# Kernel optimization log

Hardware: AMD Instinct MI355X
Metric: run time of the kernel (lower is better)

The kernel has to match this reference:

```python
import jax, jax.numpy as jnp
import numpy as np

N, E = 50000, 800000
IN, HID, LAT = 512, 256, 128


def setup_inputs() -> dict:
    key = jax.random.key(0)
    ks = jax.random.split(key, 9)
    x = jax.random.normal(ks[0], (N, IN), dtype=jnp.float32)
    edge_index = jax.random.randint(ks[1], (2, E), 0, N, dtype=jnp.int64)
    edge_attr = jax.random.uniform(ks[2], (E,), dtype=jnp.float32)
    # GCNConv weights (glorot-ish scaling) and biases
    W1 = jax.random.normal(ks[3], (IN, HID), dtype=jnp.float32) / np.sqrt(IN)
    b1 = jnp.zeros((HID,), dtype=jnp.float32)
    W_mu = jax.random.normal(ks[4], (HID, LAT), dtype=jnp.float32) / np.sqrt(HID)
    b_mu = jnp.zeros((LAT,), dtype=jnp.float32)
    W_lv = jax.random.normal(ks[5], (HID, LAT), dtype=jnp.float32) / np.sqrt(HID)
    b_lv = jnp.zeros((LAT,), dtype=jnp.float32)
    return {"x": x, "edge_index": edge_index, "edge_attr": edge_attr,
            "W1": W1, "b1": b1, "W_mu": W_mu, "b_mu": b_mu,
            "W_lv": W_lv, "b_lv": b_lv}


def _gcn_norm(edge_index, edge_attr, num_nodes):
    # GCNConv default: add self-loops (weight 1), symmetric normalization
    loops = jnp.arange(num_nodes, dtype=edge_index.dtype)
    src = jnp.concatenate([edge_index[0], loops])
    dst = jnp.concatenate([edge_index[1], loops])
    w = jnp.concatenate([edge_attr, jnp.ones((num_nodes,), edge_attr.dtype)])
    deg = jax.ops.segment_sum(w, dst, num_segments=num_nodes)
    dis = jnp.where(deg > 0, jax.lax.rsqrt(jnp.maximum(deg, 1e-12)), 0.0)
    norm = dis[src] * w * dis[dst]  # [E + N]
    return src, dst, norm


def reference(x, edge_index, edge_attr, W1, b1, W_mu, b_mu, W_lv, b_lv):
    num_nodes = x.shape[0]
    src, dst, norm = _gcn_norm(edge_index, edge_attr, num_nodes)

    def conv(h, W, b):
        m = h @ W                      # dense transform [N, out]
        msg = m[src] * norm[:, None]   # gather + scale  [E+N, out]
        return jax.ops.segment_sum(msg, dst, num_segments=num_nodes) + b

    hidden = jax.nn.relu(conv(x, W1, b1))
    # Dropout(0.2) is identity in eval mode
    mu = conv(hidden, W_mu, b_mu)
    logvar = conv(hidden, W_lv, b_lv)
    return (mu, logvar)
```

## Files before the change

kernel.cpp:

```cpp
#include <hip/hip_runtime.h>

#define IN_F 512
#define HID_F 256
#define LAT_F 128

typedef __bf16 bf16x8 __attribute__((ext_vector_type(8)));
typedef float floatx4 __attribute__((ext_vector_type(4)));

#define FIX_SCALE 1048576.0f

__device__ __forceinline__ unsigned short f2bf(float f) {
    union { float f; unsigned u; } v; v.f = f;
    unsigned r = (v.u + 0x7fff + ((v.u >> 16) & 1)) >> 16;
    return (unsigned short)r;
}
__device__ __forceinline__ float bf2f(unsigned short h) {
    union { unsigned u; float f; } v; v.u = ((unsigned)h) << 16;
    return v.f;
}

__device__ __forceinline__ void gload_lds16(const void* g, void* lds) {
    __builtin_amdgcn_global_load_lds(
        (const __attribute__((address_space(1))) unsigned int*)(uintptr_t)g,
        (__attribute__((address_space(3))) unsigned int*)(uintptr_t)lds,
        16, 0, 0);
}


__global__ void prep_all(const float* __restrict__ W1, const float* __restrict__ Wmu,
                         const float* __restrict__ Wlv, unsigned long long* __restrict__ packed,
                         unsigned short* __restrict__ W1t, unsigned short* __restrict__ B2t,
                         int N) {
    int t = blockIdx.x * 256 + threadIdx.x;
    if (t < N) packed[t] = (1ULL << 32) | (unsigned long long)(unsigned)FIX_SCALE;
    if (t < HID_F * IN_F) {
        int n = t >> 9, k = t & 511;
        W1t[t] = f2bf(W1[(size_t)k * HID_F + n]);
    }
    if (t < HID_F * HID_F) {
        int n = t >> 8, k = t & 255;
        float v = (n < 128) ? Wmu[(size_t)k * LAT_F + n] : Wlv[(size_t)k * LAT_F + (n - 128)];
        B2t[t] = f2bf(v);
    }
}


__global__ void edge_deg(const int* __restrict__ ei, const float* __restrict__ attr,
                         unsigned long long* __restrict__ packed, int* __restrict__ slot, int E) {
    int e = blockIdx.x * 256 + threadIdx.x;
    if (e < E) {
        int d = ei[E + e];
        unsigned fw = __float2uint_rn(attr[e] * FIX_SCALE);
        unsigned long long old = atomicAdd(&packed[d], (1ULL << 32) | (unsigned long long)fw);
        slot[e] = (int)(old >> 32);
    }
}

__global__ void node_dis(const unsigned long long* __restrict__ packed,
                         float* __restrict__ dis, int* __restrict__ counts, int N) {
    int i = blockIdx.x * 256 + threadIdx.x;
    if (i < N) {
        unsigned long long p = packed[i];
        counts[i] = (int)(p >> 32);
        float dg = (float)(unsigned)(p & 0xffffffffu) * (1.0f / FIX_SCALE);
        dis[i] = dg > 0.f ? rsqrtf(fmaxf(dg, 1e-12f)) : 0.f;
    }
}


__global__ void scan_blocks(const int* __restrict__ counts, int* __restrict__ excl,
                            int* __restrict__ blockSums, int N) {
    __shared__ int sdata[256];
    int tid = threadIdx.x;
    int base = blockIdx.x * 1024 + tid * 4;
    int v[4]; int sum = 0;
#pragma unroll
    for (int j = 0; j < 4; ++j) { v[j] = (base + j < N) ? counts[base + j] : 0; sum += v[j]; }
    sdata[tid] = sum;
    __syncthreads();
    for (int off = 1; off < 256; off <<= 1) {
        int t = (tid >= off) ? sdata[tid - off] : 0;
        __syncthreads();
        sdata[tid] += t;
        __syncthreads();
    }
    if (tid == 255) blockSums[blockIdx.x] = sdata[255];
    int run = sdata[tid] - sum;
#pragma unroll
    for (int j = 0; j < 4; ++j) { if (base + j < N) excl[base + j] = run; run += v[j]; }
}

__global__ void scan_sums(int* blockSums, int NB) {
    __shared__ int s[64];
    int tid = threadIdx.x;
    int v = (tid < NB) ? blockSums[tid] : 0;
    s[tid] = v;
    __syncthreads();
    for (int off = 1; off < 64; off <<= 1) {
        int t = (tid >= off) ? s[tid - off] : 0;
        __syncthreads();
        s[tid] += t;
        __syncthreads();
    }
    if (tid < NB) blockSums[tid] = s[tid] - v;
}

__global__ void scan_add(int* row_ptr, const int* __restrict__ blockSums, int N, int total) {
    int tid = threadIdx.x;
    int base = blockIdx.x * 1024 + tid * 4;
    int add = blockSums[blockIdx.x];
#pragma unroll
    for (int j = 0; j < 4; ++j) if (base + j < N) row_ptr[base + j] += add;
    if (blockIdx.x == 0 && tid == 0) row_ptr[N] = total;
}


__global__ void fill_csr(const int* __restrict__ ei, const float* __restrict__ attr,
                         const int* __restrict__ slot, const float* __restrict__ dis,
                         const int* __restrict__ row_ptr,
                         int* __restrict__ col, float* __restrict__ val, int E, int N) {
    int e = blockIdx.x * 256 + threadIdx.x;
    if (e >= E + N) return;
    int s, d, sl; float w;
    if (e < E) { s = ei[e]; d = ei[E + e]; w = attr[e]; sl = slot[e]; }
    else       { s = d = e - E; w = 1.0f; sl = 0; }
    int pos = row_ptr[d] + sl;
    col[pos] = s;
    val[pos] = dis[s] * w * dis[d];
}


template <bool ABF16>
__global__ __launch_bounds__(256) void gemm_mfma(const void* __restrict__ Avoid,
                                                 const unsigned short* __restrict__ Bt,
                                                 unsigned short* __restrict__ C,
                                                 int M, int K) {
    __shared__ unsigned short As[64 * 32];
    __shared__ unsigned short Bs[256 * 32];
    int tid = threadIdx.x;
    int wave = tid >> 6, lane = tid & 63;
    int mrow = lane & 15, quad = lane >> 4;
    int blockRow = blockIdx.x * 64;

    floatx4 acc[4][4];
#pragma unroll
    for (int i = 0; i < 4; ++i)
#pragma unroll
        for (int j = 0; j < 4; ++j) acc[i][j] = (floatx4){0.f, 0.f, 0.f, 0.f};

    int r = tid >> 2;
    int kq = tid & 3;
    int arow = blockRow + r; if (arow >= M) arow = M - 1;

    unsigned short* AsWaveBase = &As[wave * 512];

    for (int k0 = 0; k0 < K; k0 += 32) {
        if constexpr (ABF16) {
            const unsigned short* A = (const unsigned short*)Avoid;
            gload_lds16(A + (size_t)arow * K + k0 + kq * 8, AsWaveBase);
        } else {
            const float* A = (const float*)Avoid;
            const float* p = A + (size_t)arow * K + k0 + kq * 8;
            float4 a0 = *(const float4*)p, a1 = *(const float4*)(p + 4);
            unsigned short h[8] = {f2bf(a0.x), f2bf(a0.y), f2bf(a0.z), f2bf(a0.w),
                                   f2bf(a1.x), f2bf(a1.y), f2bf(a1.z), f2bf(a1.w)};
            *(uint4*)&As[r * 32 + kq * 8] = *(uint4*)h;
        }
#pragma unroll
        for (int pass = 0; pass < 4; ++pass) {
            int bcol = r + pass * 64;
            gload_lds16(Bt + (size_t)bcol * K + k0 + kq * 8,
                        &Bs[(pass * 256 + wave * 64) * 8]);
        }
        __syncthreads();
        bf16x8 af[4];
#pragma unroll
        for (int i = 0; i < 4; ++i)
            af[i] = *(const bf16x8*)&As[(i * 16 + mrow) * 32 + quad * 8];
#pragma unroll
        for (int j = 0; j < 4; ++j) {
            bf16x8 bf = *(const bf16x8*)&Bs[(wave * 64 + j * 16 + mrow) * 32 + quad * 8];
#pragma unroll
            for (int i = 0; i < 4; ++i)
                acc[i][j] = __builtin_amdgcn_mfma_f32_16x16x32_bf16(af[i], bf, acc[i][j], 0, 0, 0);
        }
        __syncthreads();
    }
#pragma unroll
    for (int i = 0; i < 4; ++i)
#pragma unroll
        for (int j = 0; j < 4; ++j) {
            int colo = wave * 64 + j * 16 + mrow;
#pragma unroll
            for (int v = 0; v < 4; ++v) {
                int row = blockRow + i * 16 + quad * 4 + v;
                if (row < M) C[(size_t)row * HID_F + colo] = f2bf(acc[i][j][v]);
            }
        }
}


__global__ void agg_relu(const unsigned short* __restrict__ m, const int* __restrict__ row_ptr,
                         const int* __restrict__ col, const float* __restrict__ val,
                         const float* __restrict__ bias, unsigned short* __restrict__ hidden) {
    int i = blockIdx.x, l = threadIdx.x, c0 = l << 2;
    int p0 = row_ptr[i], p1 = row_ptr[i + 1];
    float a0 = 0.f, a1 = 0.f, a2 = 0.f, a3 = 0.f;
    for (int p = p0; p < p1; ++p) {
        int s = col[p]; float w = val[p];
        ushort4 u = *(const ushort4*)(m + (size_t)s * HID_F + c0);
        a0 = fmaf(bf2f(u.x), w, a0);
        a1 = fmaf(bf2f(u.y), w, a1);
        a2 = fmaf(bf2f(u.z), w, a2);
        a3 = fmaf(bf2f(u.w), w, a3);
    }
    float4 b = *(const float4*)(bias + c0);
    a0 = fmaxf(a0 + b.x, 0.f); a1 = fmaxf(a1 + b.y, 0.f);
    a2 = fmaxf(a2 + b.z, 0.f); a3 = fmaxf(a3 + b.w, 0.f);
    ushort4 o = make_ushort4(f2bf(a0), f2bf(a1), f2bf(a2), f2bf(a3));
    *(ushort4*)(hidden + (size_t)i * HID_F + c0) = o;
}

__global__ void agg_out(const unsigned short* __restrict__ m, const int* __restrict__ row_ptr,
                        const int* __restrict__ col, const float* __restrict__ val,
                        const float* __restrict__ bmu, const float* __restrict__ blv,
                        float* __restrict__ out, int N) {
    int i = blockIdx.x, l = threadIdx.x, c0 = l << 2;
    int p0 = row_ptr[i], p1 = row_ptr[i + 1];
    float a0 = 0.f, a1 = 0.f, a2 = 0.f, a3 = 0.f;
    for (int p = p0; p < p1; ++p) {
        int s = col[p]; float w = val[p];
        ushort4 u = *(const ushort4*)(m + (size_t)s * HID_F + c0);
        a0 = fmaf(bf2f(u.x), w, a0);
        a1 = fmaf(bf2f(u.y), w, a1);
        a2 = fmaf(bf2f(u.z), w, a2);
        a3 = fmaf(bf2f(u.w), w, a3);
    }
    if (l < 32) {
        float4 b = *(const float4*)(bmu + c0);
        float4 o = make_float4(a0 + b.x, a1 + b.y, a2 + b.z, a3 + b.w);
        *(float4*)(out + (size_t)i * LAT_F + c0) = o;
    } else {
        int c = c0 - 128;
        float4 b = *(const float4*)(blv + c);
        float4 o = make_float4(a0 + b.x, a1 + b.y, a2 + b.z, a3 + b.w);
        *(float4*)(out + (size_t)(N + i) * LAT_F + c) = o;
    }
}


extern "C" void kernel_launch(void* const* d_in, const int* in_sizes, int n_in,
                              void* d_out, int out_size, void* d_ws, size_t ws_size,
                              hipStream_t stream) {
    const float* x    = (const float*)d_in[0];
    const int*   ei   = (const int*)d_in[1];
    const float* attr = (const float*)d_in[2];
    const float* W1   = (const float*)d_in[3];
    const float* b1   = (const float*)d_in[4];
    const float* Wmu  = (const float*)d_in[5];
    const float* bmu  = (const float*)d_in[6];
    const float* Wlv  = (const float*)d_in[7];
    const float* blv  = (const float*)d_in[8];
    float* out = (float*)d_out;

    const int N  = in_sizes[0] / IN_F;
    const int E  = in_sizes[2];
    const int EN = E + N;

    char* w = (char*)d_ws;
    size_t off = 0;
    auto carve = [&](size_t bytes) -> void* {
        void* p = w + off; off += (bytes + 255) & ~(size_t)255; return p;
    };
    unsigned long long* packed = (unsigned long long*)carve((size_t)N * 8);
    float*          dis       = (float*)carve((size_t)N * 4);
    int*            counts    = (int*)  carve((size_t)N * 4);
    int*            row_ptr   = (int*)  carve((size_t)(N + 1) * 4);
    int*            blockSums = (int*)  carve(64 * 4);
    int*            slot      = (int*)  carve((size_t)E * 4);
    int*            col       = (int*)  carve((size_t)EN * 4);
    float*          val       = (float*)carve((size_t)EN * 4);
    unsigned short* W1t       = (unsigned short*)carve((size_t)HID_F * IN_F * 2);
    unsigned short* B2t       = (unsigned short*)carve((size_t)HID_F * HID_F * 2);
    unsigned short* m         = (unsigned short*)carve((size_t)N * HID_F * 2);
    unsigned short* hidden    = (unsigned short*)carve((size_t)N * HID_F * 2);

    prep_all<<<(HID_F * IN_F + 255) / 256, 256, 0, stream>>>(W1, Wmu, Wlv, packed, W1t, B2t, N);

    edge_deg<<<(E + 255) / 256, 256, 0, stream>>>(ei, attr, packed, slot, E);
    node_dis<<<(N + 255) / 256, 256, 0, stream>>>(packed, dis, counts, N);

    int NB = (N + 1023) / 1024;
    scan_blocks<<<NB, 256, 0, stream>>>(counts, row_ptr, blockSums, N);
    scan_sums<<<1, 64, 0, stream>>>(blockSums, NB);
    scan_add<<<NB, 256, 0, stream>>>(row_ptr, blockSums, N, EN);

    fill_csr<<<(EN + 255) / 256, 256, 0, stream>>>(ei, attr, slot, dis, row_ptr, col, val, E, N);

    int gblocks = (N + 63) / 64;
    gemm_mfma<false><<<gblocks, 256, 0, stream>>>(x, W1t, m, N, IN_F);
    agg_relu<<<N, 64, 0, stream>>>(m, row_ptr, col, val, b1, hidden);
    gemm_mfma<true><<<gblocks, 256, 0, stream>>>(hidden, B2t, m, N, HID_F);
    agg_out<<<N, 64, 0, stream>>>(m, row_ptr, col, val, bmu, blv, out, N);
}
```

Before: 440.0 us.

## Double-buffer GEMM LDS tiles and fold node_dis into scan_blocks

The MFMA GEMM now uses two LDS buffers, so the next K-slice is prefetched while the current one is consumed, which cuts one barrier per iteration. In the fp32-A path the global loads are issued early and converted to bf16 after the MFMAs, to hide load latency. Separately, the node_dis kernel is removed and its degree-to-rsqrt and count extraction work is folded into scan_blocks, dropping one launch and the counts buffer. Doubling LDS raises per-block shared memory, which can lower occupancy.

```diff
diff --git a/kernel.cpp b/kernel.cpp
--- a/kernel.cpp
+++ b/kernel.cpp
@@ -56,26 +56,25 @@
     }
 }
 
-__global__ void node_dis(const unsigned long long* __restrict__ packed,
-                         float* __restrict__ dis, int* __restrict__ counts, int N) {
-    int i = blockIdx.x * 256 + threadIdx.x;
-    if (i < N) {
-        unsigned long long p = packed[i];
-        counts[i] = (int)(p >> 32);
-        float dg = (float)(unsigned)(p & 0xffffffffu) * (1.0f / FIX_SCALE);
-        dis[i] = dg > 0.f ? rsqrtf(fmaxf(dg, 1e-12f)) : 0.f;
-    }
-}
-
-
-__global__ void scan_blocks(const int* __restrict__ counts, int* __restrict__ excl,
+
+__global__ void scan_blocks(const unsigned long long* __restrict__ packed,
+                            float* __restrict__ dis, int* __restrict__ excl,
                             int* __restrict__ blockSums, int N) {
     __shared__ int sdata[256];
     int tid = threadIdx.x;
     int base = blockIdx.x * 1024 + tid * 4;
     int v[4]; int sum = 0;
 #pragma unroll
-    for (int j = 0; j < 4; ++j) { v[j] = (base + j < N) ? counts[base + j] : 0; sum += v[j]; }
+    for (int j = 0; j < 4; ++j) {
+        int c = 0;
+        if (base + j < N) {
+            unsigned long long p = packed[base + j];
+            c = (int)(p >> 32);
+            float dg = (float)(unsigned)(p & 0xffffffffu) * (1.0f / FIX_SCALE);
+            dis[base + j] = dg > 0.f ? rsqrtf(fmaxf(dg, 1e-12f)) : 0.f;
+        }
+        v[j] = c; sum += c;
+    }
     sdata[tid] = sum;
     __syncthreads();
     for (int off = 1; off < 256; off <<= 1) {
@@ -135,13 +134,16 @@
                                                  const unsigned short* __restrict__ Bt,
                                                  unsigned short* __restrict__ C,
                                                  int M, int K) {
-    __shared__ unsigned short As[64 * 32];
-    __shared__ unsigned short Bs[256 * 32];
+    __shared__ unsigned short As[2][64 * 32];
+    __shared__ unsigned short Bs[2][256 * 32];
     int tid = threadIdx.x;
     int wave = tid >> 6, lane = tid & 63;
     int mrow = lane & 15, quad = lane >> 4;
     int blockRow = blockIdx.x * 64;
 
+    const unsigned short* Abf = (const unsigned short*)Avoid;
+    const float*          Afp = (const float*)Avoid;
+
     floatx4 acc[4][4];
 #pragma unroll
     for (int i = 0; i < 4; ++i)
@@ -152,39 +154,55 @@
     int kq = tid & 3;
     int arow = blockRow + r; if (arow >= M) arow = M - 1;
 
-    unsigned short* AsWaveBase = &As[wave * 512];
-
+    if constexpr (ABF16) {
+        gload_lds16(Abf + (size_t)arow * K + kq * 8, &As[0][wave * 512]);
+    } else {
+        const float* p = Afp + (size_t)arow * K + kq * 8;
+        float4 a0 = *(const float4*)p, a1 = *(const float4*)(p + 4);
+        unsigned short h[8] = {f2bf(a0.x), f2bf(a0.y), f2bf(a0.z), f2bf(a0.w),
+                               f2bf(a1.x), f2bf(a1.y), f2bf(a1.z), f2bf(a1.w)};
+        *(uint4*)&As[0][r * 32 + kq * 8] = *(uint4*)h;
+    }
+#pragma unroll
+    for (int pass = 0; pass < 4; ++pass)
+        gload_lds16(Bt + (size_t)(r + pass * 64) * K + kq * 8,
+                    &Bs[0][(pass * 256 + wave * 64) * 8]);
+
+    int cur = 0;
     for (int k0 = 0; k0 < K; k0 += 32) {
-        if constexpr (ABF16) {
-            const unsigned short* A = (const unsigned short*)Avoid;
-            gload_lds16(A + (size_t)arow * K + k0 + kq * 8, AsWaveBase);
-        } else {
-            const float* A = (const float*)Avoid;
-            const float* p = A + (size_t)arow * K + k0 + kq * 8;
-            float4 a0 = *(const float4*)p, a1 = *(const float4*)(p + 4);
+        __syncthreads();
+        int kn = k0 + 32;
+        bool more = kn < K;
+        float4 a0, a1;
+        if (more) {
+            if constexpr (ABF16) {
+                gload_lds16(Abf + (size_t)arow * K + kn + kq * 8, &As[cur ^ 1][wave * 512]);
+            } else {
+                const float* p = Afp + (size_t)arow * K + kn + kq * 8;
+                a0 = *(const float4*)p; a1 = *(const float4*)(p + 4);
+            }
+#pragma unroll
+            for (int pass = 0; pass < 4; ++pass)
+                gload_lds16(Bt + (size_t)(r + pass * 64) * K + kn + kq * 8,
+                            &Bs[cur ^ 1][(pass * 256 + wave * 64) * 8]);
+        }
+        bf16x8 af[4];
+#pragma unroll
+        for (int i = 0; i < 4; ++i)
+            af[i] = *(const bf16x8*)&As[cur][(i * 16 + mrow) * 32 + quad * 8];
+#pragma unroll
+        for (int j = 0; j < 4; ++j) {
+            bf16x8 bf = *(const bf16x8*)&Bs[cur][(wave * 64 + j * 16 + mrow) * 32 + quad * 8];
+#pragma unroll
+            for (int i = 0; i < 4; ++i)
+                acc[i][j] = __builtin_amdgcn_mfma_f32_16x16x32_bf16(af[i], bf, acc[i][j], 0, 0, 0);
+        }
+        if (!ABF16 && more) {
             unsigned short h[8] = {f2bf(a0.x), f2bf(a0.y), f2bf(a0.z), f2bf(a0.w),
                                    f2bf(a1.x), f2bf(a1.y), f2bf(a1.z), f2bf(a1.w)};
-            *(uint4*)&As[r * 32 + kq * 8] = *(uint4*)h;
-        }
-#pragma unroll
-        for (int pass = 0; pass < 4; ++pass) {
-            int bcol = r + pass * 64;
-            gload_lds16(Bt + (size_t)bcol * K + k0 + kq * 8,
-                        &Bs[(pass * 256 + wave * 64) * 8]);
-        }
-        __syncthreads();
-        bf16x8 af[4];
-#pragma unroll
-        for (int i = 0; i < 4; ++i)
-            af[i] = *(const bf16x8*)&As[(i * 16 + mrow) * 32 + quad * 8];
-#pragma unroll
-        for (int j = 0; j < 4; ++j) {
-            bf16x8 bf = *(const bf16x8*)&Bs[(wave * 64 + j * 16 + mrow) * 32 + quad * 8];
-#pragma unroll
-            for (int i = 0; i < 4; ++i)
-                acc[i][j] = __builtin_amdgcn_mfma_f32_16x16x32_bf16(af[i], bf, acc[i][j], 0, 0, 0);
-        }
-        __syncthreads();
+            *(uint4*)&As[cur ^ 1][r * 32 + kq * 8] = *(uint4*)h;
+        }
+        cur ^= 1;
     }
 #pragma unroll
     for (int i = 0; i < 4; ++i)
@@ -274,7 +292,6 @@
     };
     unsigned long long* packed = (unsigned long long*)carve((size_t)N * 8);
     float*          dis       = (float*)carve((size_t)N * 4);
-    int*            counts    = (int*)  carve((size_t)N * 4);
     int*            row_ptr   = (int*)  carve((size_t)(N + 1) * 4);
     int*            blockSums = (int*)  carve(64 * 4);
     int*            slot      = (int*)  carve((size_t)E * 4);
@@ -288,10 +305,9 @@
     prep_all<<<(HID_F * IN_F + 255) / 256, 256, 0, stream>>>(W1, Wmu, Wlv, packed, W1t, B2t, N);
 
     edge_deg<<<(E + 255) / 256, 256, 0, stream>>>(ei, attr, packed, slot, E);
-    node_dis<<<(N + 255) / 256, 256, 0, stream>>>(packed, dis, counts, N);
 
     int NB = (N + 1023) / 1024;
-    scan_blocks<<<NB, 256, 0, stream>>>(counts, row_ptr, blockSums, N);
+    scan_blocks<<<NB, 256, 0, stream>>>(packed, dis, row_ptr, blockSums, N);
     scan_sums<<<1, 64, 0, stream>>>(blockSums, NB);
     scan_add<<<NB, 256, 0, stream>>>(row_ptr, blockSums, N, EN);
 
```

Measured after the change: 430.7 us. -2.1%, faster.
